# Optimization experiments

Measured on AMD Instinct MI355X. Metric: run time of the kernel, lower is better.

Reference implementation:

```python
import jax, jax.numpy as jnp
import numpy as np

N = 50000      # total nodes in batch
E = 640000     # directed edges
G = 64         # graphs in batch
F_IN = 24      # node features
H = 128        # hidden dim
L = 4          # num GCN layers
BN_EPS = 1e-5


def setup_inputs() -> dict:
    key = jax.random.key(0)
    ks = jax.random.split(key, 12)
    s = 0.05  # weight init scale
    return {
        "x": jax.random.normal(ks[0], (N, F_IN), jnp.float32),
        "edge_index": jax.random.randint(ks[1], (2, E), 0, N, dtype=jnp.int32),
        "batch": jnp.sort(jax.random.randint(ks[2], (N,), 0, G, dtype=jnp.int32)),
        "W0": jax.random.normal(ks[3], (F_IN, H), jnp.float32) * s,
        "Wh": jax.random.normal(ks[4], (L - 1, H, H), jnp.float32) * s,
        "b": jnp.zeros((L, H), jnp.float32),
        "bn_gamma": jnp.ones((L, H), jnp.float32),
        "bn_beta": jnp.zeros((L, H), jnp.float32),
        "bn_mean": jax.random.normal(ks[5], (L, H), jnp.float32) * 0.01,
        "bn_var": jnp.ones((L, H), jnp.float32),
        "pool_W": jax.random.normal(ks[6], (2 * H, H), jnp.float32) * s,
        "pool_b": jnp.zeros((H,), jnp.float32),
        "out_W": jax.random.normal(ks[7], (H, H // 2), jnp.float32) * s,
        "out_b": jnp.zeros((H // 2,), jnp.float32),
    }


def reference(x, edge_index, batch, W0, Wh, b, bn_gamma, bn_beta, bn_mean,
              bn_var, pool_W, pool_b, out_W, out_b):
    n = x.shape[0]
    loop = jnp.arange(n, dtype=edge_index.dtype)
    src = jnp.concatenate([edge_index[0], loop])  # [E+N] with self-loops
    dst = jnp.concatenate([edge_index[1], loop])
    # symmetric GCN normalization: deg includes self-loops, so deg >= 1
    deg = jax.ops.segment_sum(jnp.ones_like(dst, x.dtype), dst, num_segments=n)
    dis = jax.lax.rsqrt(deg)
    coef = (dis[src] * dis[dst])[:, None]  # [E+N, 1]

    def gcn_conv(h, W, bias):
        h = h @ W                                   # [N, H]
        msg = h[src] * coef                         # gather + scale
        return jax.ops.segment_sum(msg, dst, num_segments=n) + bias

    Ws = [W0] + [Wh[i] for i in range(Wh.shape[0])]
    h = x
    for i in range(L):
        h = gcn_conv(h, Ws[i], b[i])
        # BatchNorm1d (eval mode) + ReLU; dropout = identity in eval
        h = (h - bn_mean[i]) * jax.lax.rsqrt(bn_var[i] + BN_EPS) * bn_gamma[i] + bn_beta[i]
        h = jax.nn.relu(h)

    counts = jax.ops.segment_sum(jnp.ones((n,), h.dtype), batch, num_segments=G)
    x_mean = jax.ops.segment_sum(h, batch, num_segments=G) / jnp.maximum(counts, 1.0)[:, None]
    x_max = jax.ops.segment_max(h, batch, num_segments=G)
    x_pooled = jnp.concatenate([x_mean, x_max], axis=1)        # [G, 2H]
    x_pooled = jax.nn.relu(x_pooled @ pool_W + pool_b)         # global_pool MLP
    return x_pooled @ out_W + out_b                            # embedding head [G, H//2]
```

## Files before the change

### kernel.cpp

```cpp
#include <hip/hip_runtime.h>
#include <hip/hip_bf16.h>
#include <hip/hip_fp16.h>

#define HD 128
#define BN_EPS 1e-5f
#define PSPLIT 16

typedef __attribute__((ext_vector_type(8))) short short8;
typedef __attribute__((ext_vector_type(8))) _Float16 half8;
typedef __attribute__((ext_vector_type(4))) float f32x4;

__device__ inline unsigned short f2bf(float v, float& rem) {
    unsigned u = __float_as_uint(v);
    unsigned r = (u + 0x7FFFu + ((u >> 16) & 1u)) >> 16;
    rem = v - __uint_as_float(r << 16);
    return (unsigned short)r;
}

__global__ void k_count(const int* __restrict__ dst, int* __restrict__ counts, int E) {
    int i = blockIdx.x * blockDim.x + threadIdx.x;
    for (; i < E; i += gridDim.x * blockDim.x)
        atomicAdd(&counts[dst[i]], 1);
}

__global__ void k_scan1(const int* __restrict__ counts, int* __restrict__ offs,
                        int* __restrict__ bsums, int n) {
    __shared__ int s[256];
    int t = threadIdx.x, i = blockIdx.x * 256 + t;
    int v = (i < n) ? counts[i] : 0;
    s[t] = v; __syncthreads();
    for (int d = 1; d < 256; d <<= 1) {
        int x = (t >= d) ? s[t - d] : 0;
        __syncthreads(); s[t] += x; __syncthreads();
    }
    if (i < n) offs[i] = s[t] - v;
    if (t == 255) bsums[blockIdx.x] = s[255];
}

__global__ void k_scan2(int* __restrict__ bsums, int nb,
                        const int* __restrict__ batch, int* __restrict__ starts,
                        int n, int G) {
    __shared__ int s[256];
    int t = threadIdx.x;
    int v = (t < nb) ? bsums[t] : 0;
    s[t] = v; __syncthreads();
    for (int d = 1; d < 256; d <<= 1) {
        int x = (t >= d) ? s[t - d] : 0;
        __syncthreads(); s[t] += x; __syncthreads();
    }
    if (t < nb) bsums[t] = s[t] - v;
    if (t <= G) {
        int lo = 0, hi = n;
        while (lo < hi) {
            int mid = (lo + hi) >> 1;
            if (batch[mid] < t) lo = mid + 1; else hi = mid;
        }
        starts[t] = lo;
    }
}

__global__ void k_scan3(int* __restrict__ offs, const int* __restrict__ bsums,
                        int* __restrict__ cursor, const int* __restrict__ counts,
                        float* __restrict__ dis, int n) {
    int i = blockIdx.x * 256 + threadIdx.x;
    if (i < n) {
        int v = offs[i] + bsums[blockIdx.x];
        offs[i] = v;
        cursor[i] = v;
        dis[i] = rsqrtf((float)(counts[i] + 1));
    }
}

__global__ void k_fill(const int* __restrict__ src, const int* __restrict__ dst,
                       int* __restrict__ cursor, unsigned short* __restrict__ esrc, int E) {
    int i = blockIdx.x * blockDim.x + threadIdx.x;
    for (; i < E; i += gridDim.x * blockDim.x) {
        int s = src[i], d = dst[i];
        int pos = atomicAdd(&cursor[d], 1);
        esrc[pos] = (unsigned short)s;
    }
}

__global__ void k_wsplit(const float* __restrict__ W0, const float* __restrict__ Wh,
                         unsigned short* __restrict__ whi0, unsigned short* __restrict__ wlo0,
                         unsigned short* __restrict__ whf, unsigned short* __restrict__ wlf) {
    int idx = blockIdx.x * 256 + threadIdx.x;
    int l = idx >> 14, rest = idx & 16383;
    int k = rest >> 7, c = rest & 127;
    int cb = c >> 4, kc = k >> 5;
    int lane = (c & 15) | (((k & 31) >> 3) << 4);
    int j = k & 7;
    if (l == 0) {
        if (k >= 32) return;
        float val = (k < 24) ? W0[k * HD + c] : 0.f;
        float rem, rem2;
        unsigned short hi = f2bf(val, rem);
        unsigned short lo = f2bf(rem, rem2);
        size_t addr = (size_t)(cb * 64 + lane) * 8 + j;
        whi0[addr] = hi; wlo0[addr] = lo;
    } else {
        float val = Wh[(size_t)(l - 1) * HD * HD + (size_t)k * HD + c];
        __half h = __float2half(val);
        float rem = val - __half2float(h);
        __half lo = __float2half(rem);
        size_t addr = (size_t)(l - 1) * 16384 + (size_t)((cb * 4 + kc) * 64 + lane) * 8 + j;
        whf[addr] = __half_as_ushort(h);
        wlf[addr] = __half_as_ushort(lo);
    }
}

__global__ void k_agg_x(const float* __restrict__ in, const int* __restrict__ offs,
                        const int* __restrict__ counts, const unsigned short* __restrict__ esrc,
                        const float* __restrict__ dis, unsigned short* __restrict__ ohi,
                        unsigned short* __restrict__ olo, int n) {
    const int FQ = 6, GRP = 8;
    int grp = threadIdx.x / GRP;
    int lane = threadIdx.x % GRP;
    int node = blockIdx.x * (blockDim.x / GRP) + grp;
    if (node >= n) return;
    int rowblk = node >> 4, rr = node & 15;

    if (lane == FQ) {
        size_t base = (size_t)rowblk * 512 + (size_t)(rr + 48) * 8;
        ushort4 z = make_ushort4(0, 0, 0, 0);
        *(ushort4*)(ohi + base) = z; *(ushort4*)(ohi + base + 4) = z;
        *(ushort4*)(olo + base) = z; *(ushort4*)(olo + base + 4) = z;
    }
    if (lane >= FQ) return;

    const float4* in4 = reinterpret_cast<const float4*>(in);
    float dn = dis[node];
    float sl = dn * dn;
    float4 a = in4[(size_t)node * FQ + lane];
    float4 accA = make_float4(sl * a.x, sl * a.y, sl * a.z, sl * a.w);
    float4 accB = make_float4(0.f, 0.f, 0.f, 0.f);

    int e = offs[node], end = e + counts[node];
    for (; e + 3 < end; e += 4) {
        int s0 = esrc[e],     s1 = esrc[e + 1];
        int s2 = esrc[e + 2], s3 = esrc[e + 3];
        float c0 = dis[s0] * dn, c1 = dis[s1] * dn;
        float c2 = dis[s2] * dn, c3 = dis[s3] * dn;
        float4 v0 = in4[(size_t)s0 * FQ + lane];
        float4 v1 = in4[(size_t)s1 * FQ + lane];
        float4 v2 = in4[(size_t)s2 * FQ + lane];
        float4 v3 = in4[(size_t)s3 * FQ + lane];
        accA.x = fmaf(c0, v0.x, fmaf(c2, v2.x, accA.x));
        accA.y = fmaf(c0, v0.y, fmaf(c2, v2.y, accA.y));
        accA.z = fmaf(c0, v0.z, fmaf(c2, v2.z, accA.z));
        accA.w = fmaf(c0, v0.w, fmaf(c2, v2.w, accA.w));
        accB.x = fmaf(c1, v1.x, fmaf(c3, v3.x, accB.x));
        accB.y = fmaf(c1, v1.y, fmaf(c3, v3.y, accB.y));
        accB.z = fmaf(c1, v1.z, fmaf(c3, v3.z, accB.z));
        accB.w = fmaf(c1, v1.w, fmaf(c3, v3.w, accB.w));
    }
    for (; e < end; ++e) {
        int s0 = esrc[e];
        float c0 = dis[s0] * dn;
        float4 v0 = in4[(size_t)s0 * FQ + lane];
        accA.x = fmaf(c0, v0.x, accA.x);
        accA.y = fmaf(c0, v0.y, accA.y);
        accA.z = fmaf(c0, v0.z, accA.z);
        accA.w = fmaf(c0, v0.w, accA.w);
    }
    float4 acc = make_float4(accA.x + accB.x, accA.y + accB.y,
                             accA.z + accB.z, accA.w + accB.w);

    int f0 = lane * 4;
    int lidx = rr | (((f0 & 31) >> 3) << 4);
    int j0 = f0 & 7;
    size_t base = (size_t)rowblk * 512 + (size_t)lidx * 8 + j0;
    float r0, r1, r2, r3, d0;
    ushort4 hi, lo;
    hi.x = f2bf(acc.x, r0); hi.y = f2bf(acc.y, r1);
    hi.z = f2bf(acc.z, r2); hi.w = f2bf(acc.w, r3);
    lo.x = f2bf(r0, d0); lo.y = f2bf(r1, d0);
    lo.z = f2bf(r2, d0); lo.w = f2bf(r3, d0);
    *(ushort4*)(ohi + base) = hi;
    *(ushort4*)(olo + base) = lo;
}

__global__ void k_agg_h(const __half* __restrict__ in, const int* __restrict__ offs,
                        const int* __restrict__ counts, const unsigned short* __restrict__ esrc,
                        const float* __restrict__ dis, unsigned short* __restrict__ af, int n) {
    int grp = threadIdx.x >> 5;
    int lane = threadIdx.x & 31;
    int node = blockIdx.x * 8 + grp;
    if (node >= n) return;
    int rowblk = node >> 4, rr = node & 15;

    const float2* in8 = reinterpret_cast<const float2*>(in);
    float dn = dis[node];
    float sl = dn * dn;

    float2 raw = in8[(size_t)node * 32 + lane];
    __half2 p0 = *(__half2*)&raw.x, p1 = *(__half2*)&raw.y;
    float2 f0v = __half22float2(p0), f1v = __half22float2(p1);
    float4 accA = make_float4(sl * f0v.x, sl * f0v.y, sl * f1v.x, sl * f1v.y);
    float4 accB = make_float4(0.f, 0.f, 0.f, 0.f);

    int e = offs[node], end = e + counts[node];
    for (; e + 3 < end; e += 4) {
        int s0 = esrc[e],     s1 = esrc[e + 1];
        int s2 = esrc[e + 2], s3 = esrc[e + 3];
        float c0 = dis[s0] * dn, c1 = dis[s1] * dn;
        float c2 = dis[s2] * dn, c3 = dis[s3] * dn;
        float2 w0 = in8[(size_t)s0 * 32 + lane];
        float2 w1 = in8[(size_t)s1 * 32 + lane];
        float2 w2 = in8[(size_t)s2 * 32 + lane];
        float2 w3 = in8[(size_t)s3 * 32 + lane];
        float2 a0 = __half22float2(*(__half2*)&w0.x), b0 = __half22float2(*(__half2*)&w0.y);
        float2 a1 = __half22float2(*(__half2*)&w1.x), b1 = __half22float2(*(__half2*)&w1.y);
        float2 a2 = __half22float2(*(__half2*)&w2.x), b2 = __half22float2(*(__half2*)&w2.y);
        float2 a3 = __half22float2(*(__half2*)&w3.x), b3 = __half22float2(*(__half2*)&w3.y);
        accA.x = fmaf(c0, a0.x, fmaf(c2, a2.x, accA.x));
        accA.y = fmaf(c0, a0.y, fmaf(c2, a2.y, accA.y));
        accA.z = fmaf(c0, b0.x, fmaf(c2, b2.x, accA.z));
        accA.w = fmaf(c0, b0.y, fmaf(c2, b2.y, accA.w));
        accB.x = fmaf(c1, a1.x, fmaf(c3, a3.x, accB.x));
        accB.y = fmaf(c1, a1.y, fmaf(c3, a3.y, accB.y));
        accB.z = fmaf(c1, b1.x, fmaf(c3, b3.x, accB.z));
        accB.w = fmaf(c1, b1.y, fmaf(c3, b3.y, accB.w));
    }
    for (; e < end; ++e) {
        int s0 = esrc[e];
        float c0 = dis[s0] * dn;
        float2 w0 = in8[(size_t)s0 * 32 + lane];
        float2 a0 = __half22float2(*(__half2*)&w0.x), b0 = __half22float2(*(__half2*)&w0.y);
        accA.x = fmaf(c0, a0.x, accA.x);
        accA.y = fmaf(c0, a0.y, accA.y);
        accA.z = fmaf(c0, b0.x, accA.z);
        accA.w = fmaf(c0, b0.y, accA.w);
    }
    float4 acc = make_float4(accA.x + accB.x, accA.y + accB.y,
                             accA.z + accB.z, accA.w + accB.w);

    int f0 = lane * 4;
    int kc = f0 >> 5;
    int lidx = rr | (((f0 & 31) >> 3) << 4);
    int j0 = f0 & 7;
    size_t base = ((size_t)rowblk * 4 + kc) * 512 + (size_t)lidx * 8 + j0;
    ushort4 hv;
    hv.x = __half_as_ushort(__float2half(acc.x));
    hv.y = __half_as_ushort(__float2half(acc.y));
    hv.z = __half_as_ushort(__float2half(acc.z));
    hv.w = __half_as_ushort(__float2half(acc.w));
    *(ushort4*)(af + base) = hv;
}

__global__ __launch_bounds__(256) void k_gemm_m(
        const unsigned short* __restrict__ agh, const unsigned short* __restrict__ agl,
        const unsigned short* __restrict__ wh, const unsigned short* __restrict__ wl,
        const float* __restrict__ bias, const float* __restrict__ gamma,
        const float* __restrict__ beta, const float* __restrict__ mean,
        const float* __restrict__ var, __half* __restrict__ outh, int n) {
    __shared__ unsigned short lbh[8 * 512];
    __shared__ unsigned short lbl[8 * 512];
    int tid = threadIdx.x;
    for (int i = tid; i < 1024; i += 256) {
        ((ushort4*)lbh)[i] = ((const ushort4*)wh)[i];
        ((ushort4*)lbl)[i] = ((const ushort4*)wl)[i];
    }
    __syncthreads();

    int wave = tid >> 6, lane = tid & 63;
    int grb0 = blockIdx.x * 8 + wave * 2;

    f32x4 acc[2][8] = {};

    short8 a0h = *(const short8*)(agh + (size_t)grb0 * 512 + lane * 8);
    short8 a0l = *(const short8*)(agl + (size_t)grb0 * 512 + lane * 8);
    short8 a1h = *(const short8*)(agh + (size_t)(grb0 + 1) * 512 + lane * 8);
    short8 a1l = *(const short8*)(agl + (size_t)(grb0 + 1) * 512 + lane * 8);
    #pragma unroll
    for (int cb = 0; cb < 8; ++cb) {
        short8 bh = *(const short8*)(lbh + (size_t)(cb * 64 + lane) * 8);
        short8 bl = *(const short8*)(lbl + (size_t)(cb * 64 + lane) * 8);
        acc[0][cb] = __builtin_amdgcn_mfma_f32_16x16x32_bf16(a0h, bh, acc[0][cb], 0, 0, 0);
        acc[0][cb] = __builtin_amdgcn_mfma_f32_16x16x32_bf16(a0h, bl, acc[0][cb], 0, 0, 0);
        acc[0][cb] = __builtin_amdgcn_mfma_f32_16x16x32_bf16(a0l, bh, acc[0][cb], 0, 0, 0);
        acc[1][cb] = __builtin_amdgcn_mfma_f32_16x16x32_bf16(a1h, bh, acc[1][cb], 0, 0, 0);
        acc[1][cb] = __builtin_amdgcn_mfma_f32_16x16x32_bf16(a1h, bl, acc[1][cb], 0, 0, 0);
        acc[1][cb] = __builtin_amdgcn_mfma_f32_16x16x32_bf16(a1l, bh, acc[1][cb], 0, 0, 0);
    }

    int colbase = lane & 15;
    float scv[8], shv[8];
    #pragma unroll
    for (int cb = 0; cb < 8; ++cb) {
        int c = cb * 16 + colbase;
        float s = gamma[c] * rsqrtf(var[c] + BN_EPS);
        scv[cb] = s;
        shv[cb] = beta[c] + (bias[c] - mean[c]) * s;
    }
    int r0 = (lane >> 4) * 4;
    #pragma unroll
    for (int rb = 0; rb < 2; ++rb) {
        int rowb = (grb0 + rb) * 16 + r0;
        #pragma unroll
        for (int rg = 0; rg < 4; ++rg) {
            int row = rowb + rg;
            if (row < n) {
                #pragma unroll
                for (int cb = 0; cb < 8; ++cb) {
                    float v = fmaxf(fmaf(acc[rb][cb][rg], scv[cb], shv[cb]), 0.f);
                    outh[(size_t)row * HD + cb * 16 + colbase] = __float2half(v);
                }
            }
        }
    }
}

template<bool OUT_F16>
__global__ __launch_bounds__(256) void k_gemm_h(
        const unsigned short* __restrict__ af,
        const unsigned short* __restrict__ wh, const unsigned short* __restrict__ wl,
        const float* __restrict__ bias, const float* __restrict__ gamma,
        const float* __restrict__ beta, const float* __restrict__ mean,
        const float* __restrict__ var, float* __restrict__ outf,
        __half* __restrict__ outh, int n) {
    __shared__ unsigned short lbh[16384];
    __shared__ unsigned short lbl[16384];
    int tid = threadIdx.x;
    for (int i = tid; i < 4096; i += 256) {
        ((ushort4*)lbh)[i] = ((const ushort4*)wh)[i];
        ((ushort4*)lbl)[i] = ((const ushort4*)wl)[i];
    }
    __syncthreads();

    int wave = tid >> 6, lane = tid & 63;
    int grb0 = blockIdx.x * 8 + wave * 2;

    f32x4 acc[2][8] = {};

    #pragma unroll
    for (int kc = 0; kc < 4; ++kc) {
        half8 a0 = *(const half8*)(af + ((size_t)grb0 * 4 + kc) * 512 + lane * 8);
        half8 a1 = *(const half8*)(af + ((size_t)(grb0 + 1) * 4 + kc) * 512 + lane * 8);
        #pragma unroll
        for (int cb = 0; cb < 8; ++cb) {
            half8 bh = *(const half8*)(lbh + (size_t)((cb * 4 + kc) * 64 + lane) * 8);
            half8 bl = *(const half8*)(lbl + (size_t)((cb * 4 + kc) * 64 + lane) * 8);
            acc[0][cb] = __builtin_amdgcn_mfma_f32_16x16x32_f16(a0, bh, acc[0][cb], 0, 0, 0);
            acc[0][cb] = __builtin_amdgcn_mfma_f32_16x16x32_f16(a0, bl, acc[0][cb], 0, 0, 0);
            acc[1][cb] = __builtin_amdgcn_mfma_f32_16x16x32_f16(a1, bh, acc[1][cb], 0, 0, 0);
            acc[1][cb] = __builtin_amdgcn_mfma_f32_16x16x32_f16(a1, bl, acc[1][cb], 0, 0, 0);
        }
    }

    int colbase = lane & 15;
    float scv[8], shv[8];
    #pragma unroll
    for (int cb = 0; cb < 8; ++cb) {
        int c = cb * 16 + colbase;
        float s = gamma[c] * rsqrtf(var[c] + BN_EPS);
        scv[cb] = s;
        shv[cb] = beta[c] + (bias[c] - mean[c]) * s;
    }
    int r0 = (lane >> 4) * 4;
    #pragma unroll
    for (int rb = 0; rb < 2; ++rb) {
        int rowb = (grb0 + rb) * 16 + r0;
        #pragma unroll
        for (int rg = 0; rg < 4; ++rg) {
            int row = rowb + rg;
            if (row < n) {
                #pragma unroll
                for (int cb = 0; cb < 8; ++cb) {
                    float v = fmaxf(fmaf(acc[rb][cb][rg], scv[cb], shv[cb]), 0.f);
                    if (OUT_F16)
                        outh[(size_t)row * HD + cb * 16 + colbase] = __float2half(v);
                    else
                        outf[(size_t)row * HD + cb * 16 + colbase] = v;
                }
            }
        }
    }
}

__global__ void k_pool(const float* __restrict__ h, const int* __restrict__ starts,
                       float* __restrict__ gsum, unsigned int* __restrict__ gmax) {
    int g = blockIdx.x;
    int slice = blockIdx.y;
    int t = threadIdx.x;
    int s = starts[g], e = starts[g + 1];
    int cnt = e - s;
    int per = (cnt + PSPLIT - 1) / PSPLIT;
    int beg = s + slice * per;
    int end = min(beg + per, e);
    if (beg >= end) return;
    float sum = 0.f, mx = 0.f;
    for (int node = beg; node < end; ++node) {
        float v = h[(size_t)node * HD + t];
        sum += v;
        mx = fmaxf(mx, v);
    }
    atomicAdd(&gsum[g * HD + t], sum);
    atomicMax(&gmax[g * HD + t], __float_as_uint(mx));
}

__global__ void k_head(const float* __restrict__ gsum, const unsigned int* __restrict__ gmax,
                       const int* __restrict__ starts, const float* __restrict__ pool_W,
                       const float* __restrict__ pool_b, const float* __restrict__ out_W,
                       const float* __restrict__ out_b, float* __restrict__ out) {
    int g = blockIdx.x, t = threadIdx.x;
    __shared__ float pooled[2 * HD];
    __shared__ float hid_s[HD];
    float cntf = fmaxf((float)(starts[g + 1] - starts[g]), 1.f);
    pooled[t] = gsum[g * HD + t] / cntf;
    pooled[HD + t] = __uint_as_float(gmax[g * HD + t]);
    __syncthreads();
    float acc = pool_b[t];
    for (int k = 0; k < 2 * HD; ++k)
        acc += pooled[k] * pool_W[k * HD + t];
    hid_s[t] = fmaxf(acc, 0.f);
    __syncthreads();
    if (t < 64) {
        float a2 = out_b[t];
        for (int j = 0; j < HD; ++j)
            a2 += hid_s[j] * out_W[j * 64 + t];
        out[g * 64 + t] = a2;
    }
}

extern "C" void kernel_launch(void* const* d_in, const int* in_sizes, int n_in,
                              void* d_out, int out_size, void* d_ws, size_t ws_size,
                              hipStream_t stream) {
    const float* x        = (const float*)d_in[0];
    const int*   eidx     = (const int*)d_in[1];
    const int*   batch    = (const int*)d_in[2];
    const float* W0       = (const float*)d_in[3];
    const float* Wh       = (const float*)d_in[4];
    const float* b        = (const float*)d_in[5];
    const float* bn_gamma = (const float*)d_in[6];
    const float* bn_beta  = (const float*)d_in[7];
    const float* bn_mean  = (const float*)d_in[8];
    const float* bn_var   = (const float*)d_in[9];
    const float* pool_W   = (const float*)d_in[10];
    const float* pool_b   = (const float*)d_in[11];
    const float* out_W    = (const float*)d_in[12];
    const float* out_b    = (const float*)d_in[13];
    float* out = (float*)d_out;

    const int N = in_sizes[2];
    const int E = in_sizes[1] / 2;
    const int L = in_sizes[5] / HD;
    const int G = out_size / (HD / 2);

    const int* src = eidx;
    const int* dst = eidx + E;

    const int NBLK = (N + 127) / 128;
    const size_t NRB = (size_t)NBLK * 8;

    char* p = (char*)d_ws;
    float*  h    = (float*)p;  p += (size_t)N * HD * 4;
    __half* hf   = (__half*)p; p += (size_t)NBLK * 128 * HD * 2;
    unsigned short* af  = (unsigned short*)p; p += NRB * 4 * 512 * 2;
    unsigned short* agh = (unsigned short*)p; p += NRB * 512 * 2;
    unsigned short* agl = (unsigned short*)p; p += NRB * 512 * 2;
    unsigned short* whi0 = (unsigned short*)p; p += (size_t)16384 * 2;
    unsigned short* wlo0 = (unsigned short*)p; p += (size_t)16384 * 2;
    unsigned short* whf  = (unsigned short*)p; p += (size_t)3 * 16384 * 2;
    unsigned short* wlf  = (unsigned short*)p; p += (size_t)3 * 16384 * 2;
    unsigned short* esrc = (unsigned short*)p; p += (((size_t)E * 2 + 15) & ~15ull);
    int*   counts  = (int*)p;   p += (size_t)N * 4;
    float* dis     = (float*)p; p += (size_t)N * 4;
    int*   offs    = (int*)p;   p += (size_t)(N + 1) * 4;
    int*   cursor  = (int*)p;   p += (size_t)N * 4;
    int*   bsums   = (int*)p;   p += 256 * 4;
    float* gsum    = (float*)p; p += (size_t)G * HD * 4;
    unsigned int* gmax = (unsigned int*)p; p += (size_t)G * HD * 4;
    int*   starts  = (int*)p;   p += (size_t)(G + 1) * 4;
    (void)ws_size; (void)n_in;

    hipMemsetAsync(counts, 0, (size_t)N * 4, stream);
    hipMemsetAsync(gsum, 0, (size_t)G * HD * 8, stream);

    const int NB = (N + 255) / 256;

    k_count<<<1024, 256, 0, stream>>>(dst, counts, E);
    k_scan1<<<NB, 256, 0, stream>>>(counts, offs, bsums, N);
    k_scan2<<<1, 256, 0, stream>>>(bsums, NB, batch, starts, N, G);
    k_scan3<<<NB, 256, 0, stream>>>(offs, bsums, cursor, counts, dis, N);
    k_fill<<<1024, 256, 0, stream>>>(src, dst, cursor, esrc, E);
    k_wsplit<<<256, 256, 0, stream>>>(W0, Wh, whi0, wlo0, whf, wlf);

    k_agg_x<<<(N + 31) / 32, 256, 0, stream>>>(x, offs, counts, esrc, dis, agh, agl, N);
    k_gemm_m<<<NBLK, 256, 0, stream>>>(agh, agl, whi0, wlo0, b, bn_gamma, bn_beta,
                                       bn_mean, bn_var, hf, N);

    for (int l = 1; l < L; ++l) {
        k_agg_h<<<(N + 7) / 8, 256, 0, stream>>>(hf, offs, counts, esrc, dis, af, N);
        const unsigned short* wh_l = whf + (size_t)(l - 1) * 16384;
        const unsigned short* wl_l = wlf + (size_t)(l - 1) * 16384;
        if (l < L - 1)
            k_gemm_h<true><<<NBLK, 256, 0, stream>>>(af, wh_l, wl_l,
                b + l * HD, bn_gamma + l * HD, bn_beta + l * HD,
                bn_mean + l * HD, bn_var + l * HD, nullptr, hf, N);
        else
            k_gemm_h<false><<<NBLK, 256, 0, stream>>>(af, wh_l, wl_l,
                b + l * HD, bn_gamma + l * HD, bn_beta + l * HD,
                bn_mean + l * HD, bn_var + l * HD, h, nullptr, N);
    }

    dim3 pgrid(G, PSPLIT);
    k_pool<<<pgrid, HD, 0, stream>>>(h, starts, gsum, gmax);
    k_head<<<G, HD, 0, stream>>>(gsum, gmax, starts, pool_W, pool_b, out_W, out_b, out);
}
```

Measured before the change: 279.8 us.

## Fuse graph pooling into last GEMM epilogue and drop CSR fill atomics

The final GCN layer's GEMM epilogue now reduces sum and max per graph in LDS and flushes them with global atomics, so the separate pooling kernel and the fp32 hidden-state write and read are removed. Separately, the count kernel records each edge's slot within its destination bucket, so the fill kernel computes positions directly instead of taking a second round of atomics on a cursor array. This adds LDS atomics, extra barriers in the last GEMM and an extra ordinal buffer. Storing the slot as a 16-bit value assumes no node has more than 65535 incoming edges.

```diff
diff --git a/kernel.cpp b/kernel.cpp
--- a/kernel.cpp
+++ b/kernel.cpp
@@ -4,7 +4,6 @@
 
 #define HD 128
 #define BN_EPS 1e-5f
-#define PSPLIT 16
 
 typedef __attribute__((ext_vector_type(8))) short short8;
 typedef __attribute__((ext_vector_type(8))) _Float16 half8;
@@ -17,10 +16,13 @@
     return (unsigned short)r;
 }
 
-__global__ void k_count(const int* __restrict__ dst, int* __restrict__ counts, int E) {
+__global__ void k_count(const int* __restrict__ dst, int* __restrict__ counts,
+                        unsigned short* __restrict__ ord, int E) {
     int i = blockIdx.x * blockDim.x + threadIdx.x;
-    for (; i < E; i += gridDim.x * blockDim.x)
-        atomicAdd(&counts[dst[i]], 1);
+    for (; i < E; i += gridDim.x * blockDim.x) {
+        int pos = atomicAdd(&counts[dst[i]], 1);
+        ord[i] = (unsigned short)pos;
+    }
 }
 
 __global__ void k_scan1(const int* __restrict__ counts, int* __restrict__ offs,
@@ -60,24 +62,21 @@
 }
 
 __global__ void k_scan3(int* __restrict__ offs, const int* __restrict__ bsums,
-                        int* __restrict__ cursor, const int* __restrict__ counts,
-                        float* __restrict__ dis, int n) {
+                        const int* __restrict__ counts, float* __restrict__ dis, int n) {
     int i = blockIdx.x * 256 + threadIdx.x;
     if (i < n) {
-        int v = offs[i] + bsums[blockIdx.x];
-        offs[i] = v;
-        cursor[i] = v;
+        offs[i] += bsums[blockIdx.x];
         dis[i] = rsqrtf((float)(counts[i] + 1));
     }
 }
 
 __global__ void k_fill(const int* __restrict__ src, const int* __restrict__ dst,
-                       int* __restrict__ cursor, unsigned short* __restrict__ esrc, int E) {
+                       const unsigned short* __restrict__ ord, const int* __restrict__ offs,
+                       unsigned short* __restrict__ esrc, int E) {
     int i = blockIdx.x * blockDim.x + threadIdx.x;
     for (; i < E; i += gridDim.x * blockDim.x) {
         int s = src[i], d = dst[i];
-        int pos = atomicAdd(&cursor[d], 1);
-        esrc[pos] = (unsigned short)s;
+        esrc[offs[d] + ord[i]] = (unsigned short)s;
     }
 }
 
@@ -311,14 +310,15 @@
     }
 }
 
-template<bool OUT_F16>
+template<bool POOL>
 __global__ __launch_bounds__(256) void k_gemm_h(
         const unsigned short* __restrict__ af,
         const unsigned short* __restrict__ wh, const unsigned short* __restrict__ wl,
         const float* __restrict__ bias, const float* __restrict__ gamma,
         const float* __restrict__ beta, const float* __restrict__ mean,
-        const float* __restrict__ var, float* __restrict__ outf,
-        __half* __restrict__ outh, int n) {
+        const float* __restrict__ var, __half* __restrict__ outh,
+        const int* __restrict__ batch, float* __restrict__ gsum,
+        unsigned int* __restrict__ gmax, int n) {
     __shared__ unsigned short lbh[16384];
     __shared__ unsigned short lbl[16384];
     int tid = threadIdx.x;
@@ -358,45 +358,79 @@
         shv[cb] = beta[c] + (bias[c] - mean[c]) * s;
     }
     int r0 = (lane >> 4) * 4;
-    #pragma unroll
-    for (int rb = 0; rb < 2; ++rb) {
-        int rowb = (grb0 + rb) * 16 + r0;
+
+    if (!POOL) {
         #pragma unroll
-        for (int rg = 0; rg < 4; ++rg) {
-            int row = rowb + rg;
-            if (row < n) {
-                #pragma unroll
-                for (int cb = 0; cb < 8; ++cb) {
-                    float v = fmaxf(fmaf(acc[rb][cb][rg], scv[cb], shv[cb]), 0.f);
-                    if (OUT_F16)
+        for (int rb = 0; rb < 2; ++rb) {
+            int rowb = (grb0 + rb) * 16 + r0;
+            #pragma unroll
+            for (int rg = 0; rg < 4; ++rg) {
+                int row = rowb + rg;
+                if (row < n) {
+                    #pragma unroll
+                    for (int cb = 0; cb < 8; ++cb) {
+                        float v = fmaxf(fmaf(acc[rb][cb][rg], scv[cb], shv[cb]), 0.f);
                         outh[(size_t)row * HD + cb * 16 + colbase] = __float2half(v);
-                    else
-                        outf[(size_t)row * HD + cb * 16 + colbase] = v;
+                    }
                 }
             }
         }
-    }
-}
-
-__global__ void k_pool(const float* __restrict__ h, const int* __restrict__ starts,
-                       float* __restrict__ gsum, unsigned int* __restrict__ gmax) {
-    int g = blockIdx.x;
-    int slice = blockIdx.y;
-    int t = threadIdx.x;
-    int s = starts[g], e = starts[g + 1];
-    int cnt = e - s;
-    int per = (cnt + PSPLIT - 1) / PSPLIT;
-    int beg = s + slice * per;
-    int end = min(beg + per, e);
-    if (beg >= end) return;
-    float sum = 0.f, mx = 0.f;
-    for (int node = beg; node < end; ++node) {
-        float v = h[(size_t)node * HD + t];
-        sum += v;
-        mx = fmaxf(mx, v);
-    }
-    atomicAdd(&gsum[g * HD + t], sum);
-    atomicMax(&gmax[g * HD + t], __float_as_uint(mx));
+    } else {
+        int row0 = blockIdx.x * 128;
+        int row_hi = min(n - 1, row0 + 127);
+        int g_lo = batch[row0];
+        int g_hi = batch[row_hi];
+
+        int gval[2][4];
+        #pragma unroll
+        for (int rb = 0; rb < 2; ++rb) {
+            int rowb = (grb0 + rb) * 16 + r0;
+            #pragma unroll
+            for (int rg = 0; rg < 4; ++rg) {
+                int row = rowb + rg;
+                gval[rb][rg] = (row < n) ? batch[row] : -1;
+            }
+        }
+
+        __syncthreads();
+        float* lds_sum = reinterpret_cast<float*>(lbh);
+        unsigned int* lds_max = reinterpret_cast<unsigned int*>(lbh) + 512;
+
+        for (int gbase = g_lo; gbase <= g_hi; gbase += 4) {
+            for (int i = tid; i < 512; i += 256) {
+                lds_sum[i] = 0.f;
+                lds_max[i] = 0u;
+            }
+            __syncthreads();
+            #pragma unroll
+            for (int rb = 0; rb < 2; ++rb) {
+                #pragma unroll
+                for (int rg = 0; rg < 4; ++rg) {
+                    int g = gval[rb][rg];
+                    if (g >= gbase && g < gbase + 4) {
+                        int sbase = (g - gbase) * 128;
+                        #pragma unroll
+                        for (int cb = 0; cb < 8; ++cb) {
+                            float v = fmaxf(fmaf(acc[rb][cb][rg], scv[cb], shv[cb]), 0.f);
+                            int col = cb * 16 + colbase;
+                            atomicAdd(&lds_sum[sbase + col], v);
+                            atomicMax(&lds_max[sbase + col], __float_as_uint(v));
+                        }
+                    }
+                }
+            }
+            __syncthreads();
+            for (int i = tid; i < 512; i += 256) {
+                int s = i >> 7, col = i & 127;
+                int g = gbase + s;
+                if (g <= g_hi) {
+                    atomicAdd(&gsum[g * HD + col], lds_sum[i]);
+                    atomicMax(&gmax[g * HD + col], lds_max[i]);
+                }
+            }
+            __syncthreads();
+        }
+    }
 }
 
 __global__ void k_head(const float* __restrict__ gsum, const unsigned int* __restrict__ gmax,
@@ -454,7 +488,6 @@
     const size_t NRB = (size_t)NBLK * 8;
 
     char* p = (char*)d_ws;
-    float*  h    = (float*)p;  p += (size_t)N * HD * 4;
     __half* hf   = (__half*)p; p += (size_t)NBLK * 128 * HD * 2;
     unsigned short* af  = (unsigned short*)p; p += NRB * 4 * 512 * 2;
     unsigned short* agh = (unsigned short*)p; p += NRB * 512 * 2;
@@ -464,10 +497,10 @@
     unsigned short* whf  = (unsigned short*)p; p += (size_t)3 * 16384 * 2;
     unsigned short* wlf  = (unsigned short*)p; p += (size_t)3 * 16384 * 2;
     unsigned short* esrc = (unsigned short*)p; p += (((size_t)E * 2 + 15) & ~15ull);
+    unsigned short* ord  = (unsigned short*)p; p += (((size_t)E * 2 + 15) & ~15ull);
     int*   counts  = (int*)p;   p += (size_t)N * 4;
     float* dis     = (float*)p; p += (size_t)N * 4;
     int*   offs    = (int*)p;   p += (size_t)(N + 1) * 4;
-    int*   cursor  = (int*)p;   p += (size_t)N * 4;
     int*   bsums   = (int*)p;   p += 256 * 4;
     float* gsum    = (float*)p; p += (size_t)G * HD * 4;
     unsigned int* gmax = (unsigned int*)p; p += (size_t)G * HD * 4;
@@ -479,11 +512,11 @@
 
     const int NB = (N + 255) / 256;
 
-    k_count<<<1024, 256, 0, stream>>>(dst, counts, E);
+    k_count<<<1024, 256, 0, stream>>>(dst, counts, ord, E);
     k_scan1<<<NB, 256, 0, stream>>>(counts, offs, bsums, N);
     k_scan2<<<1, 256, 0, stream>>>(bsums, NB, batch, starts, N, G);
-    k_scan3<<<NB, 256, 0, stream>>>(offs, bsums, cursor, counts, dis, N);
-    k_fill<<<1024, 256, 0, stream>>>(src, dst, cursor, esrc, E);
+    k_scan3<<<NB, 256, 0, stream>>>(offs, bsums, counts, dis, N);
+    k_fill<<<1024, 256, 0, stream>>>(src, dst, ord, offs, esrc, E);
     k_wsplit<<<256, 256, 0, stream>>>(W0, Wh, whi0, wlo0, whf, wlf);
 
     k_agg_x<<<(N + 31) / 32, 256, 0, stream>>>(x, offs, counts, esrc, dis, agh, agl, N);
@@ -495,16 +528,14 @@
         const unsigned short* wh_l = whf + (size_t)(l - 1) * 16384;
         const unsigned short* wl_l = wlf + (size_t)(l - 1) * 16384;
         if (l < L - 1)
+            k_gemm_h<false><<<NBLK, 256, 0, stream>>>(af, wh_l, wl_l,
+                b + l * HD, bn_gamma + l * HD, bn_beta + l * HD,
+                bn_mean + l * HD, bn_var + l * HD, hf, batch, gsum, gmax, N);
+        else
             k_gemm_h<true><<<NBLK, 256, 0, stream>>>(af, wh_l, wl_l,
                 b + l * HD, bn_gamma + l * HD, bn_beta + l * HD,
-                bn_mean + l * HD, bn_var + l * HD, nullptr, hf, N);
-        else
-            k_gemm_h<false><<<NBLK, 256, 0, stream>>>(af, wh_l, wl_l,
-                b + l * HD, bn_gamma + l * HD, bn_beta + l * HD,
-                bn_mean + l * HD, bn_var + l * HD, h, nullptr, N);
-    }
-
-    dim3 pgrid(G, PSPLIT);
-    k_pool<<<pgrid, HD, 0, stream>>>(h, starts, gsum, gmax);
+                bn_mean + l * HD, bn_var + l * HD, nullptr, batch, gsum, gmax, N);
+    }
+
     k_head<<<G, HD, 0, stream>>>(gsum, gmax, starts, pool_W, pool_b, out_W, out_b, out);
 }
```

Result: no change. 275.0 us (-1.7%).
